# Performance work log

Hardware: AMD Instinct MI355X
Metric: run time of the kernel (lower is better)

The kernel has to match this reference:

```python
import jax, jax.numpy as jnp
import numpy as np
import math

N_LAYERS = 2
N_HEADS = 8
D_MODEL = 512
D_FF = 2048
B = 2
L = 2048
GELU_C = 0.7978845608028654  # sqrt(2/pi)
LN_EPS = 1e-5


def gelu_tanh(x):
    # faithful to the module's custom GELU: 0.5*x*(1+tanh(sqrt(2/pi)*(x+0.044715*x^3)))
    return 0.5 * x * (1.0 + jnp.tanh(GELU_C * (x + 0.044715 * x * x * x)))


def layernorm(x, g, b):
    m = jnp.mean(x, axis=-1, keepdims=True)
    v = jnp.mean((x - m) ** 2, axis=-1, keepdims=True)
    return (x - m) * jax.lax.rsqrt(v + LN_EPS) * g + b


def setup_inputs() -> dict:
    key = jax.random.key(0)
    ks = jax.random.split(key, 24)
    w = lambda k, shape: jax.random.normal(k, shape, dtype=jnp.float32) * 0.02
    inp = {
        "x": jax.random.normal(ks[0], (B, L, D_MODEL), dtype=jnp.float32),
        # tau is exp(tau_learner(...)) in the full model -> positive scalar per batch
        "tau": jax.random.uniform(ks[1], (B, 1), dtype=jnp.float32) + 0.5,
        "delta": jax.random.normal(ks[2], (B, L), dtype=jnp.float32) * 0.1,
        # NStransformer builds an upper-triangular causal mask (True = masked)
        "att_mask": jnp.triu(jnp.ones((L, L), dtype=bool), k=1),
        "Wq": w(ks[3], (N_LAYERS, D_MODEL, D_MODEL)), "bq": jnp.zeros((N_LAYERS, D_MODEL), jnp.float32),
        "Wk": w(ks[4], (N_LAYERS, D_MODEL, D_MODEL)), "bk": jnp.zeros((N_LAYERS, D_MODEL), jnp.float32),
        "Wv": w(ks[5], (N_LAYERS, D_MODEL, D_MODEL)), "bv": jnp.zeros((N_LAYERS, D_MODEL), jnp.float32),
        "Wo": w(ks[6], (N_LAYERS, D_MODEL, D_MODEL)), "bo": jnp.zeros((N_LAYERS, D_MODEL), jnp.float32),
        # conv1/conv2 are kernel_size=1 Conv1d == pointwise linears
        "W1": w(ks[7], (N_LAYERS, D_MODEL, D_FF)), "b1": jnp.zeros((N_LAYERS, D_FF), jnp.float32),
        "W2": w(ks[8], (N_LAYERS, D_FF, D_MODEL)), "b2": jnp.zeros((N_LAYERS, D_MODEL), jnp.float32),
        "ln1_g": jnp.ones((N_LAYERS, D_MODEL), jnp.float32), "ln1_b": jnp.zeros((N_LAYERS, D_MODEL), jnp.float32),
        "ln2_g": jnp.ones((N_LAYERS, D_MODEL), jnp.float32), "ln2_b": jnp.zeros((N_LAYERS, D_MODEL), jnp.float32),
        "lnf_g": jnp.ones((D_MODEL,), jnp.float32), "lnf_b": jnp.zeros((D_MODEL,), jnp.float32),
    }
    return inp


def reference(x, tau, delta, att_mask, Wq, bq, Wk, bk, Wv, bv, Wo, bo,
              W1, b1, W2, b2, ln1_g, ln1_b, ln2_g, ln2_b, lnf_g, lnf_b):
    Bsz, Ls, D = x.shape
    H = N_HEADS
    E = D // H
    scale = 1.0 / math.sqrt(E)
    t = tau[:, None, None, :]    # (B,1) -> (B,1,1,1)
    d = delta[:, None, None, :]  # (B,L) -> (B,1,1,L)
    neg_inf = jnp.float32(-jnp.inf)
    for l in range(N_LAYERS):
        q = (x @ Wq[l] + bq[l]).reshape(Bsz, Ls, H, E)
        k = (x @ Wk[l] + bk[l]).reshape(Bsz, Ls, H, E)
        v = (x @ Wv[l] + bv[l]).reshape(Bsz, Ls, H, E)
        # de-stationary scores: QK^T * tau + delta, then masked softmax
        scores = jnp.einsum('blhe,bshe->bhls', q, k) * t + d  # (B,H,L,S)
        scores = jnp.where(att_mask, neg_inf, scores)
        A = jax.nn.softmax(scale * scores, axis=-1)  # dropout is identity in eval
        V = jnp.einsum('bhls,bshd->blhd', A, v).reshape(Bsz, Ls, D)
        x = (V @ Wo[l] + bo[l]) + x
        xb = layernorm(x, ln1_g[l], ln1_b[l])
        h = gelu_tanh(xb @ W1[l] + b1[l])   # conv1 (k=1)
        o = h @ W2[l] + b2[l]               # conv2 (k=1)
        x = layernorm(o + xb, ln2_g[l], ln2_b[l])
    return layernorm(x, lnf_g, lnf_b)
```

## Files before the change

### kernel.cpp

```cpp
#include <hip/hip_runtime.h>
#include <stdint.h>

#define DM   512
#define DFF  2048
#define NH   8
#define EH   64
#define SEQ  2048
#define NBAT 2
#define NTOK (NBAT*SEQ)
#define LOG2E 1.44269504088896340736f

typedef __attribute__((ext_vector_type(8))) short  s16x8;
typedef __attribute__((ext_vector_type(8))) __bf16 bf16x8;
typedef __attribute__((ext_vector_type(4))) float  f32x4;

__device__ __forceinline__ short f2bf(float f) {
  union { float f; unsigned int i; } c; c.f = f;
  unsigned int x = c.i;
  x += 0x7fffu + ((x >> 16) & 1u);
  return (short)(x >> 16);
}
__device__ __forceinline__ float bf2f(short u) {
  union { unsigned int i; float f; } c;
  c.i = ((unsigned int)(unsigned short)u) << 16;
  return c.f;
}
__device__ __forceinline__ f32x4 mfma16(bf16x8 a, bf16x8 b, f32x4 c) {
  return __builtin_amdgcn_mfma_f32_16x16x32_bf16(a, b, c, 0, 0, 0);
}
__device__ __forceinline__ void gl_lds16(const short* g, short* l) {
  __builtin_amdgcn_global_load_lds(
      (const __attribute__((address_space(1))) unsigned int*)(const void*)g,
      (__attribute__((address_space(3))) unsigned int*)(void*)l, 16, 0, 0);
}

__global__ __launch_bounds__(256) void fill_code_f32(float* __restrict__ out,
                                                     float code)
{
  out[blockIdx.x * 256 + threadIdx.x] = code;
}

__global__ __launch_bounds__(256) void prep_weights(
    const float* __restrict__ Wq, const float* __restrict__ Wk,
    const float* __restrict__ Wv, const float* __restrict__ Wo,
    const float* __restrict__ W1, const float* __restrict__ W2,
    short* __restrict__ Wqkvt, short* __restrict__ Wot,
    short* __restrict__ W1t,   short* __restrict__ W2t)
{
  int gw   = blockIdx.x * 4 + (threadIdx.x >> 6);
  int lane = threadIdx.x & 63;
  int l = gw / 6144;
  int g = gw % 6144;
  const float* src; short* dst; int K, N, gi;
  if (g < 2048) {
    int w = g >> 9; gi = g & 511; K = 512; N = 512;
    src = (w == 0 ? Wq : w == 1 ? Wk : w == 2 ? Wv : Wo) + l * 262144;
    dst = (w < 3) ? (Wqkvt + l * 786432 + w * 262144) : (Wot + l * 262144);
  } else if (g < 4096) {
    gi = g - 2048; K = 512; N = 2048;
    src = W1 + l * 1048576; dst = W1t + l * 1048576;
  } else {
    gi = g - 4096; K = 2048; N = 512;
    src = W2 + l * 1048576; dst = W2t + l * 1048576;
  }
  int nb = N >> 6;
  int n  = (gi % nb) * 64 + lane;
  int k0 = (gi / nb) * 8;
  s16x8 v;
  #pragma unroll
  for (int i = 0; i < 8; i++) v[i] = f2bf(src[(size_t)(k0 + i) * N + n]);
  *(s16x8*)(dst + (size_t)n * K + k0) = v;
}

__global__ __launch_bounds__(256) void cast_kernel(const float* __restrict__ in,
                                                   float* __restrict__ outf,
                                                   short* __restrict__ outb)
{
  int i = blockIdx.x * 256 + threadIdx.x;
  float v = in[i];
  outf[i] = v;
  outb[i] = f2bf(v);
}

__global__ __launch_bounds__(256) void skred(
    const short* __restrict__ parts, const float* __restrict__ bias,
    const float* __restrict__ rf, const short* __restrict__ rb,
    float* __restrict__ of)
{
  const int g = blockIdx.x * 256 + threadIdx.x;
  const size_t base = (size_t)g * 8;
  float s[8];
  #pragma unroll
  for (int j = 0; j < 8; j++) s[j] = bias[(base + j) & 511];
  #pragma unroll
  for (int p = 0; p < 4; p++) {
    s16x8 v = *(const s16x8*)(parts + (size_t)p * 2097152 + base);
    #pragma unroll
    for (int j = 0; j < 8; j++) s[j] += bf2f(v[j]);
  }
  if (rf) {
    #pragma unroll
    for (int j = 0; j < 8; j++) s[j] += rf[base + j];
  } else {
    s16x8 v = *(const s16x8*)(rb + base);
    #pragma unroll
    for (int j = 0; j < 8; j++) s[j] += bf2f(v[j]);
  }
  #pragma unroll
  for (int j = 0; j < 8; j++) of[base + j] = s[j];
}

template<int TM>
__global__ __launch_bounds__(256) void gemm_bt(
    const short* __restrict__ A, const short* __restrict__ Bt,
    int M, int N, int K, int KS, int mode,
    const float* __restrict__ bq, const float* __restrict__ bk,
    const float* __restrict__ bv,
    short* __restrict__ oq, short* __restrict__ okk, short* __restrict__ ov)
{
  __shared__ short As[TM * 32];
  __shared__ short Bs[128 * 32];
  constexpr int MT = TM / 32;
  const int tid  = threadIdx.x;
  const int lane = tid & 63;
  const int wid  = tid >> 6;
  const int lm   = lane & 15, quad = lane >> 4;
  const int nbn  = N >> 7;
  const int nb2  = (M / TM) * nbn;
  const int ks   = blockIdx.x / nb2;
  const int rem  = blockIdx.x % nb2;
  const int m0   = (rem / nbn) * TM;
  const int n0   = (rem % nbn) << 7;
  const int wm   = (wid & 1) * (TM / 2), wn = (wid >> 1) * 64;
  const int Kc   = K / KS;
  const int kbeg = ks * Kc;

  f32x4 acc[MT][4];
  #pragma unroll
  for (int i = 0; i < MT; i++)
    #pragma unroll
    for (int j = 0; j < 4; j++) acc[i][j] = (f32x4){0.f, 0.f, 0.f, 0.f};

  const short* Abase = A  + (size_t)m0 * K;
  const short* Bbase = Bt + (size_t)n0 * K;

  for (int k0 = kbeg; k0 < kbeg + Kc; k0 += 32) {
    __syncthreads();
    #pragma unroll
    for (int j = 0; j < TM / 64; j++) {
      int c = j * 256 + wid * 64 + lane;
      gl_lds16(Abase + (size_t)(c >> 2) * K + k0 + (c & 3) * 8,
               &As[(j * 256 + wid * 64) * 8]);
    }
    #pragma unroll
    for (int j = 0; j < 2; j++) {
      int c = j * 256 + wid * 64 + lane;
      gl_lds16(Bbase + (size_t)(c >> 2) * K + k0 + (c & 3) * 8,
               &Bs[(j * 256 + wid * 64) * 8]);
    }
    __syncthreads();
    bf16x8 af[MT], bfr[4];
    #pragma unroll
    for (int t = 0; t < MT; t++)
      af[t] = *(const bf16x8*)&As[(wm + t * 16 + lm) * 32 + quad * 8];
    #pragma unroll
    for (int t = 0; t < 4; t++)
      bfr[t] = *(const bf16x8*)&Bs[(wn + t * 16 + lm) * 32 + quad * 8];
    #pragma unroll
    for (int mt = 0; mt < MT; mt++)
      #pragma unroll
      for (int nt = 0; nt < 4; nt++)
        acc[mt][nt] = mfma16(af[mt], bfr[nt], acc[mt][nt]);
  }

  #pragma unroll
  for (int mt = 0; mt < MT; mt++) {
    int row = m0 + wm + mt * 16 + quad * 4;
    #pragma unroll
    for (int nt = 0; nt < 4; nt++) {
      int col = n0 + wn + nt * 16 + lm;
      f32x4 v = acc[mt][nt];
      if (mode == 0) {
        int which = col >> 9; int d = col & 511;
        int hh = d >> 6; int e = d & 63;
        const float* bias = which == 0 ? bq : which == 1 ? bk : bv;
        float bb = bias[d];
        #pragma unroll
        for (int r = 0; r < 4; r++) {
          int tok = row + r; int bI = tok >> 11, li = tok & 2047;
          float val = v[r] + bb;
          if (which == 0)
            oq [(((size_t)bI * NH + hh) * SEQ + li) * EH + e] = f2bf(val);
          else if (which == 1)
            okk[(((size_t)bI * NH + hh) * SEQ + li) * EH + e] = f2bf(val);
          else
            ov [(((size_t)bI * NH + hh) * EH + e) * SEQ + li] = f2bf(val);
        }
      } else if (mode == 2) {
        float bb = bq[col];
        #pragma unroll
        for (int r = 0; r < 4; r++) {
          float x = v[r] + bb;
          float u = 0.7978845608f * (x + 0.044715f * x * x * x);
          float t = 1.f - 2.f / (1.f + __expf(2.f * u));
          size_t idx = (size_t)(row + r) * N + col;
          oq[idx] = f2bf(0.5f * x * (1.f + t));
        }
      } else {
        short* op = oq + (size_t)ks * M * N;
        #pragma unroll
        for (int r = 0; r < 4; r++)
          op[(size_t)(row + r) * N + col] = f2bf(v[r]);
      }
    }
  }
}

__global__ __launch_bounds__(256) void attn_v7(
    const short* __restrict__ Q, const short* __restrict__ Kg,
    const short* __restrict__ Vt,
    const float* __restrict__ tau, const float* __restrict__ delta,
    short* __restrict__ opart, float* __restrict__ lpart)
{
  __shared__ short Ks[64 * 72];
  __shared__ short Vs[64 * 72];
  __shared__ short Ps[4][16 * 72];
  const int tid  = threadIdx.x;
  const int lane = tid & 63, wid = tid >> 6;
  const int lm = lane & 15, quad = lane >> 4;
  const int t    = blockIdx.x >> 2;
  const int part = blockIdx.x & 3;
  const int qb = 31 - (t & 31);
  const int h  = (t >> 5) & 7;
  const int b  = t >> 8;
  const int q0 = qb * 64;
  const int qw = q0 + wid * 16;
  const size_t bhq = ((size_t)b * NH + h) * SEQ;
  const short* kbase = Kg + bhq * EH;
  const short* vbase = Vt + ((size_t)b * NH + h) * (size_t)(EH * SEQ);

  const int nblk = qb + 1;
  const int kb0 = (nblk * part) >> 2;
  const int kb1 = (nblk * (part + 1)) >> 2;

  bf16x8 qf0 = *(const bf16x8*)(Q + (bhq + qw + lm) * EH + quad * 8);
  bf16x8 qf1 = *(const bf16x8*)(Q + (bhq + qw + lm) * EH + 32 + quad * 8);

  const float st2 = 0.125f * LOG2E * tau[b];
  f32x4 O[4];
  #pragma unroll
  for (int i = 0; i < 4; i++) O[i] = (f32x4){0.f, 0.f, 0.f, 0.f};
  float lr[4] = {0.f, 0.f, 0.f, 0.f};

  const int c0 = tid, c1 = tid + 256;
  const int r0 = c0 >> 3, ch0 = (c0 & 7) * 8;
  const int r1 = c1 >> 3, ch1 = (c1 & 7) * 8;

  for (int kb = kb0; kb < kb1; kb++) {
    const int s0 = kb << 6;
    s16x8 ka = *(const s16x8*)(kbase + (size_t)(s0 + r0) * EH + ch0);
    s16x8 kb_ = *(const s16x8*)(kbase + (size_t)(s0 + r1) * EH + ch1);
    s16x8 va = *(const s16x8*)(vbase + (size_t)r0 * SEQ + s0 + ch0);
    s16x8 vb = *(const s16x8*)(vbase + (size_t)r1 * SEQ + s0 + ch1);
    __syncthreads();
    *(s16x8*)&Ks[r0 * 72 + ch0] = ka;
    *(s16x8*)&Ks[r1 * 72 + ch1] = kb_;
    *(s16x8*)&Vs[r0 * 72 + ch0] = va;
    *(s16x8*)&Vs[r1 * 72 + ch1] = vb;
    __syncthreads();

    f32x4 S[4];
    #pragma unroll
    for (int nt = 0; nt < 4; nt++) {
      S[nt] = (f32x4){0.f, 0.f, 0.f, 0.f};
      S[nt] = mfma16(qf0, *(const bf16x8*)&Ks[(nt*16 + lm) * 72 + quad * 8], S[nt]);
      S[nt] = mfma16(qf1, *(const bf16x8*)&Ks[(nt*16 + lm) * 72 + 32 + quad * 8], S[nt]);
    }
    float dl[4];
    #pragma unroll
    for (int nt = 0; nt < 4; nt++)
      dl[nt] = fmaf(0.125f * LOG2E, delta[(size_t)b * SEQ + s0 + nt * 16 + lm],
                    -8.f);

    const bool diag = (kb == qb);
    #pragma unroll
    for (int r = 0; r < 4; r++) {
      float sc[4];
      #pragma unroll
      for (int nt = 0; nt < 4; nt++) sc[nt] = fmaf(st2, S[nt][r], dl[nt]);
      if (diag) {
        int rowq = qw + quad * 4 + r;
        #pragma unroll
        for (int nt = 0; nt < 4; nt++)
          if (s0 + nt * 16 + lm > rowq) sc[nt] = -__builtin_inff();
      }
      float p0 = exp2f(sc[0]), p1 = exp2f(sc[1]);
      float p2 = exp2f(sc[2]), p3 = exp2f(sc[3]);
      lr[r] += (p0 + p1) + (p2 + p3);
      short* pr = &Ps[wid][(quad * 4 + r) * 72];
      pr[lm]      = f2bf(p0);
      pr[16 + lm] = f2bf(p1);
      pr[32 + lm] = f2bf(p2);
      pr[48 + lm] = f2bf(p3);
    }

    bf16x8 pf0 = *(const bf16x8*)&Ps[wid][lm * 72 + quad * 8];
    bf16x8 pf1 = *(const bf16x8*)&Ps[wid][lm * 72 + 32 + quad * 8];
    #pragma unroll
    for (int et = 0; et < 4; et++) {
      O[et] = mfma16(pf0, *(const bf16x8*)&Vs[(et*16 + lm) * 72 + quad * 8], O[et]);
      O[et] = mfma16(pf1, *(const bf16x8*)&Vs[(et*16 + lm) * 72 + 32 + quad * 8], O[et]);
    }
  }

  #pragma unroll
  for (int r = 0; r < 4; r++) {
    float s = lr[r];
    #pragma unroll
    for (int off = 1; off < 16; off <<= 1) s += __shfl_xor(s, off);
    lr[r] = s;
  }

  const int slot = ((t << 2) | part);
  short* ob = opart + (size_t)slot * 4096;
  float* lb = lpart + (size_t)slot * 64;
  #pragma unroll
  for (int r = 0; r < 4; r++) {
    int qloc = wid * 16 + quad * 4 + r;
    #pragma unroll
    for (int et = 0; et < 4; et++)
      ob[qloc * 64 + et * 16 + lm] = f2bf(O[et][r]);
    if (lm == 0) lb[qloc] = lr[r];
  }
}

__global__ __launch_bounds__(256) void attn_reduce(
    const short* __restrict__ opart, const float* __restrict__ lpart,
    short* __restrict__ Oa)
{
  const int t = blockIdx.x;
  const int qb = 31 - (t & 31);
  const int h  = (t >> 5) & 7;
  const int b  = t >> 8;
  const int q0 = qb * 64;
  #pragma unroll
  for (int i = 0; i < 16; i++) {
    int idx = i * 256 + threadIdx.x;
    int q = idx >> 6, e = idx & 63;
    float l = 0.f, o = 0.f;
    #pragma unroll
    for (int p = 0; p < 4; p++) {
      int slot = t * 4 + p;
      l += lpart[(size_t)slot * 64 + q];
      o += bf2f(opart[(size_t)slot * 4096 + idx]);
    }
    Oa[((size_t)b * SEQ + q0 + q) * DM + h * EH + e] = f2bf(o / l);
  }
}

__global__ __launch_bounds__(256) void ln_kernel(
    const float* in, const float* __restrict__ g, const float* __restrict__ bb,
    float* outf, short* outb)
{
  int row  = blockIdx.x * 4 + (threadIdx.x >> 6);
  int lane = threadIdx.x & 63;
  const float* p = in + (size_t)row * DM;
  float v[8]; float s = 0.f, ss = 0.f;
  #pragma unroll
  for (int i = 0; i < 8; i++) {
    float x = p[lane + i * 64]; v[i] = x; s += x; ss += x * x;
  }
  #pragma unroll
  for (int off = 32; off > 0; off >>= 1) {
    s += __shfl_xor(s, off); ss += __shfl_xor(ss, off);
  }
  float mean = s * (1.f / DM);
  float var  = ss * (1.f / DM) - mean * mean;
  float rstd = rsqrtf(var + 1e-5f);
  #pragma unroll
  for (int i = 0; i < 8; i++) {
    int c = lane + i * 64;
    float y = (v[i] - mean) * rstd * g[c] + bb[c];
    if (outf) outf[(size_t)row * DM + c] = y;
    if (outb) outb[(size_t)row * DM + c] = f2bf(y);
  }
}

extern "C" void kernel_launch(void* const* d_in, const int* in_sizes, int n_in,
                              void* d_out, int out_size, void* d_ws, size_t ws_size,
                              hipStream_t stream)
{
  float* out = (float*)d_out;

  if (ws_size < (size_t)62918656) {
    fill_code_f32<<<2097152 / 256, 256, 0, stream>>>(
        out, 1200.f + (float)(ws_size >> 20));
    return;
  }

  const float* x    = (const float*)d_in[0];
  const float* tau  = (const float*)d_in[1];
  const float* del  = (const float*)d_in[2];
  const float* Wq = (const float*)d_in[4];
  const float* bq = (const float*)d_in[5];
  const float* Wk = (const float*)d_in[6];
  const float* bk = (const float*)d_in[7];
  const float* Wv = (const float*)d_in[8];
  const float* bv = (const float*)d_in[9];
  const float* Wo = (const float*)d_in[10];
  const float* bo = (const float*)d_in[11];
  const float* W1 = (const float*)d_in[12];
  const float* b1 = (const float*)d_in[13];
  const float* W2 = (const float*)d_in[14];
  const float* b2 = (const float*)d_in[15];
  const float* ln1g = (const float*)d_in[16];
  const float* ln1b = (const float*)d_in[17];
  const float* ln2g = (const float*)d_in[18];
  const float* ln2b = (const float*)d_in[19];
  const float* lnfg = (const float*)d_in[20];
  const float* lnfb = (const float*)d_in[21];

  char* ws = (char*)d_ws;
  float* sumf  = (float*)(ws + 0);
  short* x16   = (short*)(ws + 8388608);
  short* xb16  = (short*)(ws + 12582912);
  short* q16   = (short*)(ws + 16777216);
  short* k16   = (short*)(ws + 20971520);
  short* vt16  = (short*)(ws + 25165824);
  short* at16  = (short*)(ws + 29360128);
  short* h16   = (short*)(ws + 33554432);
  short* Wqkvt = (short*)(ws + 50331648);
  short* Wot   = (short*)(ws + 53477376);
  short* W1t   = (short*)(ws + 54525952);
  short* W2t   = (short*)(ws + 58720256);
  short* aopart = (short*)(ws + 33554432);
  float* alpart = (float*)(ws + 12582912);
  short* oppart = (short*)(ws + 33554432);
  short* f2part = (short*)(ws + 16777216);

  prep_weights<<<3072, 256, 0, stream>>>(Wq, Wk, Wv, Wo, W1, W2,
                                         Wqkvt, Wot, W1t, W2t);
  cast_kernel<<<NTOK * DM / 256, 256, 0, stream>>>(x, sumf, x16);

  for (int l = 0; l < 2; l++) {
    gemm_bt<64><<<64 * 12, 256, 0, stream>>>(x16, Wqkvt + l * 786432,
        NTOK, 3 * DM, DM, 1, 0,
        bq + l * DM, bk + l * DM, bv + l * DM,
        q16, k16, vt16);
    attn_v7<<<4 * NBAT * NH * (SEQ / 64), 256, 0, stream>>>(
        q16, k16, vt16, tau, del, aopart, alpart);
    attn_reduce<<<NBAT * NH * (SEQ / 64), 256, 0, stream>>>(
        aopart, alpart, at16);
    gemm_bt<64><<<64 * 4 * 4, 256, 0, stream>>>(at16, Wot + l * 262144,
        NTOK, DM, DM, 4, 4,
        nullptr, nullptr, nullptr,
        oppart, nullptr, nullptr);
    skred<<<1024, 256, 0, stream>>>(oppart, bo + l * DM, sumf, nullptr, sumf);
    ln_kernel<<<NTOK / 4, 256, 0, stream>>>(sumf, ln1g + l * DM, ln1b + l * DM,
                                            nullptr, xb16);
    gemm_bt<64><<<64 * 16, 256, 0, stream>>>(xb16, W1t + l * 1048576,
        NTOK, DFF, DM, 1, 2,
        b1 + l * DFF, nullptr, nullptr,
        h16, nullptr, nullptr);
    gemm_bt<64><<<64 * 4 * 4, 256, 0, stream>>>(h16, W2t + l * 1048576,
        NTOK, DM, DFF, 4, 4,
        nullptr, nullptr, nullptr,
        f2part, nullptr, nullptr);
    skred<<<1024, 256, 0, stream>>>(f2part, b2 + l * DM, nullptr, xb16, sumf);
    ln_kernel<<<NTOK / 4, 256, 0, stream>>>(sumf, ln2g + l * DM, ln2b + l * DM,
                                            sumf, x16);
  }
  ln_kernel<<<NTOK / 4, 256, 0, stream>>>(sumf, lnfg, lnfb, out, nullptr);
}
```

Baseline: 437.3 us.

## Fuse split-K reduction with LayerNorm, double GEMM K-step, truncate softmax probabilities

The split-K partial-sum reduction kernel now also computes LayerNorm in the same pass, with one wavefront per row and a shuffle reduction. This removes a separate LN launch and one fp32 round trip through memory. The GEMM now loads two 32-wide K slices per barrier pair, halving the number of synchronisations at the cost of twice the LDS per block. In attention, the probabilities are converted to bf16 by truncation instead of round-to-nearest, and the row sum uses the truncated values so it stays consistent. This saves ALU work but slightly changes numerics.

```diff
diff --git a/kernel.cpp b/kernel.cpp
--- a/kernel.cpp
+++ b/kernel.cpp
@@ -82,32 +82,57 @@
   outb[i] = f2bf(v);
 }
 
-__global__ __launch_bounds__(256) void skred(
+__global__ __launch_bounds__(256) void skred_ln(
     const short* __restrict__ parts, const float* __restrict__ bias,
     const float* __restrict__ rf, const short* __restrict__ rb,
-    float* __restrict__ of)
-{
-  const int g = blockIdx.x * 256 + threadIdx.x;
-  const size_t base = (size_t)g * 8;
-  float s[8];
-  #pragma unroll
-  for (int j = 0; j < 8; j++) s[j] = bias[(base + j) & 511];
+    const float* __restrict__ g, const float* __restrict__ bb,
+    float* __restrict__ sumf, short* __restrict__ outb, int mode)
+{
+  const int row  = blockIdx.x * 4 + (threadIdx.x >> 6);
+  const int lane = threadIdx.x & 63;
+  const int col  = lane * 8;
+  const size_t base = (size_t)row * DM + col;
+  float t[8];
+  #pragma unroll
+  for (int j = 0; j < 8; j++) t[j] = bias[col + j];
   #pragma unroll
   for (int p = 0; p < 4; p++) {
-    s16x8 v = *(const s16x8*)(parts + (size_t)p * 2097152 + base);
-    #pragma unroll
-    for (int j = 0; j < 8; j++) s[j] += bf2f(v[j]);
-  }
-  if (rf) {
-    #pragma unroll
-    for (int j = 0; j < 8; j++) s[j] += rf[base + j];
+    s16x8 v = *(const s16x8*)(parts + (size_t)p * (NTOK * DM) + base);
+    #pragma unroll
+    for (int j = 0; j < 8; j++) t[j] += bf2f(v[j]);
+  }
+  if (mode == 0) {
+    #pragma unroll
+    for (int j = 0; j < 8; j++) t[j] += rf[base + j];
   } else {
     s16x8 v = *(const s16x8*)(rb + base);
     #pragma unroll
-    for (int j = 0; j < 8; j++) s[j] += bf2f(v[j]);
-  }
-  #pragma unroll
-  for (int j = 0; j < 8; j++) of[base + j] = s[j];
+    for (int j = 0; j < 8; j++) t[j] += bf2f(v[j]);
+  }
+  float s = 0.f, ss = 0.f;
+  #pragma unroll
+  for (int j = 0; j < 8; j++) { s += t[j]; ss += t[j] * t[j]; }
+  #pragma unroll
+  for (int off = 32; off > 0; off >>= 1) {
+    s += __shfl_xor(s, off); ss += __shfl_xor(ss, off);
+  }
+  float mean = s * (1.f / DM);
+  float var  = ss * (1.f / DM) - mean * mean;
+  float rstd = rsqrtf(var + 1e-5f);
+  if (mode == 0) {
+    #pragma unroll
+    for (int j = 0; j < 8; j++) {
+      sumf[base + j] = t[j];
+      outb[base + j] = f2bf((t[j] - mean) * rstd * g[col + j] + bb[col + j]);
+    }
+  } else {
+    #pragma unroll
+    for (int j = 0; j < 8; j++) {
+      float y = (t[j] - mean) * rstd * g[col + j] + bb[col + j];
+      sumf[base + j] = y;
+      outb[base + j] = f2bf(y);
+    }
+  }
 }
 
 template<int TM>
@@ -118,8 +143,8 @@
     const float* __restrict__ bv,
     short* __restrict__ oq, short* __restrict__ okk, short* __restrict__ ov)
 {
-  __shared__ short As[TM * 32];
-  __shared__ short Bs[128 * 32];
+  __shared__ short As[2][TM * 32];
+  __shared__ short Bs[2][128 * 32];
   constexpr int MT = TM / 32;
   const int tid  = threadIdx.x;
   const int lane = tid & 63;
@@ -144,33 +169,40 @@
   const short* Abase = A  + (size_t)m0 * K;
   const short* Bbase = Bt + (size_t)n0 * K;
 
-  for (int k0 = kbeg; k0 < kbeg + Kc; k0 += 32) {
+  for (int k0 = kbeg; k0 < kbeg + Kc; k0 += 64) {
     __syncthreads();
     #pragma unroll
-    for (int j = 0; j < TM / 64; j++) {
-      int c = j * 256 + wid * 64 + lane;
-      gl_lds16(Abase + (size_t)(c >> 2) * K + k0 + (c & 3) * 8,
-               &As[(j * 256 + wid * 64) * 8]);
-    }
-    #pragma unroll
-    for (int j = 0; j < 2; j++) {
-      int c = j * 256 + wid * 64 + lane;
-      gl_lds16(Bbase + (size_t)(c >> 2) * K + k0 + (c & 3) * 8,
-               &Bs[(j * 256 + wid * 64) * 8]);
+    for (int half = 0; half < 2; half++) {
+      const int kk = k0 + half * 32;
+      #pragma unroll
+      for (int j = 0; j < TM / 64; j++) {
+        int c = j * 256 + wid * 64 + lane;
+        gl_lds16(Abase + (size_t)(c >> 2) * K + kk + (c & 3) * 8,
+                 &As[half][(j * 256 + wid * 64) * 8]);
+      }
+      #pragma unroll
+      for (int j = 0; j < 2; j++) {
+        int c = j * 256 + wid * 64 + lane;
+        gl_lds16(Bbase + (size_t)(c >> 2) * K + kk + (c & 3) * 8,
+                 &Bs[half][(j * 256 + wid * 64) * 8]);
+      }
     }
     __syncthreads();
-    bf16x8 af[MT], bfr[4];
-    #pragma unroll
-    for (int t = 0; t < MT; t++)
-      af[t] = *(const bf16x8*)&As[(wm + t * 16 + lm) * 32 + quad * 8];
-    #pragma unroll
-    for (int t = 0; t < 4; t++)
-      bfr[t] = *(const bf16x8*)&Bs[(wn + t * 16 + lm) * 32 + quad * 8];
-    #pragma unroll
-    for (int mt = 0; mt < MT; mt++)
+    #pragma unroll
+    for (int half = 0; half < 2; half++) {
+      bf16x8 af[MT], bfr[4];
       #pragma unroll
-      for (int nt = 0; nt < 4; nt++)
-        acc[mt][nt] = mfma16(af[mt], bfr[nt], acc[mt][nt]);
+      for (int t = 0; t < MT; t++)
+        af[t] = *(const bf16x8*)&As[half][(wm + t * 16 + lm) * 32 + quad * 8];
+      #pragma unroll
+      for (int t = 0; t < 4; t++)
+        bfr[t] = *(const bf16x8*)&Bs[half][(wn + t * 16 + lm) * 32 + quad * 8];
+      #pragma unroll
+      for (int mt = 0; mt < MT; mt++)
+        #pragma unroll
+        for (int nt = 0; nt < 4; nt++)
+          acc[mt][nt] = mfma16(af[mt], bfr[nt], acc[mt][nt]);
+    }
   }
 
   #pragma unroll
@@ -294,14 +326,19 @@
         for (int nt = 0; nt < 4; nt++)
           if (s0 + nt * 16 + lm > rowq) sc[nt] = -__builtin_inff();
       }
-      float p0 = exp2f(sc[0]), p1 = exp2f(sc[1]);
-      float p2 = exp2f(sc[2]), p3 = exp2f(sc[3]);
-      lr[r] += (p0 + p1) + (p2 + p3);
+      unsigned int u0 = __float_as_uint(exp2f(sc[0]));
+      unsigned int u1 = __float_as_uint(exp2f(sc[1]));
+      unsigned int u2 = __float_as_uint(exp2f(sc[2]));
+      unsigned int u3 = __float_as_uint(exp2f(sc[3]));
+      lr[r] += (__uint_as_float(u0 & 0xffff0000u) +
+                __uint_as_float(u1 & 0xffff0000u)) +
+               (__uint_as_float(u2 & 0xffff0000u) +
+                __uint_as_float(u3 & 0xffff0000u));
       short* pr = &Ps[wid][(quad * 4 + r) * 72];
-      pr[lm]      = f2bf(p0);
-      pr[16 + lm] = f2bf(p1);
-      pr[32 + lm] = f2bf(p2);
-      pr[48 + lm] = f2bf(p3);
+      pr[lm]      = (short)(u0 >> 16);
+      pr[16 + lm] = (short)(u1 >> 16);
+      pr[32 + lm] = (short)(u2 >> 16);
+      pr[48 + lm] = (short)(u3 >> 16);
     }
 
     bf16x8 pf0 = *(const bf16x8*)&Ps[wid][lm * 72 + quad * 8];
@@ -455,9 +492,8 @@
         NTOK, DM, DM, 4, 4,
         nullptr, nullptr, nullptr,
         oppart, nullptr, nullptr);
-    skred<<<1024, 256, 0, stream>>>(oppart, bo + l * DM, sumf, nullptr, sumf);
-    ln_kernel<<<NTOK / 4, 256, 0, stream>>>(sumf, ln1g + l * DM, ln1b + l * DM,
-                                            nullptr, xb16);
+    skred_ln<<<1024, 256, 0, stream>>>(oppart, bo + l * DM, sumf, nullptr,
+        ln1g + l * DM, ln1b + l * DM, sumf, xb16, 0);
     gemm_bt<64><<<64 * 16, 256, 0, stream>>>(xb16, W1t + l * 1048576,
         NTOK, DFF, DM, 1, 2,
         b1 + l * DFF, nullptr, nullptr,
@@ -466,9 +502,8 @@
         NTOK, DM, DFF, 4, 4,
         nullptr, nullptr, nullptr,
         f2part, nullptr, nullptr);
-    skred<<<1024, 256, 0, stream>>>(f2part, b2 + l * DM, nullptr, xb16, sumf);
-    ln_kernel<<<NTOK / 4, 256, 0, stream>>>(sumf, ln2g + l * DM, ln2b + l * DM,
-                                            sumf, x16);
+    skred_ln<<<1024, 256, 0, stream>>>(f2part, b2 + l * DM, nullptr, xb16,
+        ln2g + l * DM, ln2b + l * DM, sumf, x16, 1);
   }
   ln_kernel<<<NTOK / 4, 256, 0, stream>>>(sumf, lnfg, lnfb, out, nullptr);
 }
```

Result: faster. 405.8 us (-7.2%).
